# Optimization experiments

Hardware: AMD Instinct MI355X
Metric: run time of the kernel (lower is better)

Reference implementation:

```python
import jax, jax.numpy as jnp
import numpy as np

B, L, H, V = 64, 8, 4096, 50257


def setup_inputs() -> dict:
    key = jax.random.key(0)
    ks = jax.random.split(key, 5)
    return {
        "embedding": jax.random.normal(ks[0], (V, H), jnp.float32) * 0.02,
        "hidden_states": jax.random.normal(ks[1], (B, L, H), jnp.float32),
        "output_position": 7,  # scalar index of the position to sample from
        "temperatures": jax.random.uniform(ks[2], (B,), jnp.float32, 0.5, 1.5),
        "top_ps": jax.random.uniform(ks[3], (B,), jnp.float32, 0.7, 1.0),
        "tops_ks": jax.random.randint(ks[4], (B,), 1, 64),  # top-k in [1,64)
        "embedding_bias": jnp.zeros((V,), jnp.float32),
    }


def reference(embedding, hidden_states, output_position, temperatures, top_ps, tops_ks, embedding_bias):
    # select the output position: [B, H]
    h = hidden_states[:, output_position, :]
    # logits GEMM against tied embedding: [B, V]
    logits = jnp.einsum("bh,vh->bv", h, embedding) + embedding_bias[None, :]
    logits = logits / temperatures[:, None]
    probs = jax.nn.softmax(logits.astype(jnp.float32), axis=-1)

    # descending sort of probabilities
    order = jnp.argsort(-probs, axis=-1)                       # [B, V]
    probs_sort = jnp.take_along_axis(probs, order, axis=-1)    # [B, V]

    # top-p mask: exclusive cumulative sum exceeding top_p
    cum = jnp.cumsum(probs_sort, axis=-1)
    topp_mask = (cum - probs_sort) > top_ps[:, None]
    # top-k mask: rank >= k
    ranks = jnp.arange(V, dtype=tops_ks.dtype)[None, :]
    topk_mask = ranks >= tops_ks[:, None]

    probs_sort = jnp.where(topp_mask | topk_mask, 0.0, probs_sort)
    probs_sort = probs_sort / jnp.sum(probs_sort, axis=-1, keepdims=True)

    # scatter back to original vocab order via inverse permutation
    inv = jnp.argsort(order, axis=-1)
    probs_final = jnp.take_along_axis(probs_sort, inv, axis=-1)  # [B, V]

    # multinomial sampling (1 sample per row)
    logp = jnp.where(probs_final > 0, jnp.log(jnp.maximum(probs_final, 1e-38)), -jnp.inf)
    next_token_ids = jax.random.categorical(jax.random.key(42), logp, axis=-1)
    return next_token_ids
```

## Files before the change

### kernel.cpp

```cpp
#include <hip/hip_runtime.h>
#include <stdint.h>
#include <float.h>
#include <limits.h>


typedef __bf16 bf16x8 __attribute__((ext_vector_type(8)));
typedef float  f32x4  __attribute__((ext_vector_type(4)));

__device__ __forceinline__ void split8v(const float* f, bf16x8& hi, bf16x8& lo) {
#pragma unroll
    for (int e = 0; e < 8; ++e) {
        const __bf16 h = (__bf16)f[e];
        hi[e] = h;
        lo[e] = (__bf16)(f[e] - (float)h);
    }
}
__device__ __forceinline__ void split8(const float* f, uint4& hi, uint4& lo) {
    bf16x8 vh, vl;
    split8v(f, vh, vl);
    hi = __builtin_bit_cast(uint4, vh);
    lo = __builtin_bit_cast(uint4, vl);
}

__global__ __launch_bounds__(256) void prep_h(
    const float* __restrict__ hs, const int* __restrict__ pos_p,
    unsigned short* __restrict__ Ahi, unsigned short* __restrict__ Alo,
    int H, int L)
{
    const int pos = pos_p[0];
    const int tid = blockIdx.x * 256 + threadIdx.x;
    const int b     = tid >> 8;
    const int kbase = (tid & 255) * 16;
    const float* src = hs + ((size_t)b * L + pos) * H + kbase;
    float f[16];
    *(float4*)&f[0]  = *(const float4*)(src);
    *(float4*)&f[4]  = *(const float4*)(src + 4);
    *(float4*)&f[8]  = *(const float4*)(src + 8);
    *(float4*)&f[12] = *(const float4*)(src + 12);

    const int r16 = b >> 4, ll = b & 15;
    const int kc  = kbase >> 5;
    const int lh0 = (kbase >> 3) & 3;
#pragma unroll
    for (int c = 0; c < 2; ++c) {
        uint4 hi, lo;
        split8(f + 8 * c, hi, lo);
        const size_t dst = ((size_t)(r16 * 128 + kc) * 64 + (lh0 + c) * 16 + ll) * 8;
        *(uint4*)&Ahi[dst] = hi;
        *(uint4*)&Alo[dst] = lo;
    }
}

__global__ __launch_bounds__(256) void logits_mfma(
    const float* __restrict__ emb,
    const unsigned short* __restrict__ Ahi,
    const unsigned short* __restrict__ Alo,
    const float* __restrict__ temps,
    const float* __restrict__ bias,
    float*       __restrict__ out,
    int V, int H)
{
    const int tid  = threadIdx.x;
    const int lane = tid & 63;
    const int w    = tid >> 6;
    const int wv0  = blockIdx.x * 128 + w * 32;

    const int ll = lane & 15;
    const int lh = lane >> 4;

    const int NKC = H >> 5;

    const float* bptr[2];
#pragma unroll
    for (int n = 0; n < 2; ++n) {
        int r = wv0 + 16 * n + ll;
        r = (r < V) ? r : (V - 1);
        bptr[n] = emb + (size_t)r * H + lh * 8;
    }

    const size_t aoff = (size_t)lh * 128 + (size_t)ll * 8;

    float4 rb[4][4];
    bf16x8 aih[2][4], ail[2][4];
    f32x4  acc[4][2];
#pragma unroll
    for (int i = 0; i < 4; ++i)
#pragma unroll
        for (int j = 0; j < 2; ++j)
            acc[i][j] = (f32x4){0.f, 0.f, 0.f, 0.f};

#define LOADB(t, bi) do {                                                     \
    if ((t) < NKC) {                                                          \
        _Pragma("unroll")                                                     \
        for (int n = 0; n < 2; ++n) {                                         \
            _Pragma("unroll")                                                 \
            for (int q = 0; q < 2; ++q)                                       \
                rb[bi][n * 2 + q] =                                           \
                    *(const float4*)(bptr[n] + (size_t)(t) * 32 + q * 4);     \
        }                                                                     \
    }                                                                         \
} while (0)

#define LOADA(t, p) do {                                                      \
    if ((t) < NKC) {                                                          \
        _Pragma("unroll")                                                     \
        for (int i = 0; i < 4; ++i) {                                         \
            const size_t ai = aoff + (size_t)i * 65536 + (size_t)(t) * 512;   \
            aih[p][i] = *(const bf16x8*)&Ahi[ai];                             \
            ail[p][i] = *(const bf16x8*)&Alo[ai];                             \
        }                                                                     \
    }                                                                         \
} while (0)

#define COMPUTE(bi, p) do {                                                   \
    bf16x8 fbh[2], fbl[2];                                                    \
    _Pragma("unroll")                                                         \
    for (int n = 0; n < 2; ++n) {                                             \
        float f[8];                                                           \
        *(float4*)&f[0] = rb[bi][2 * n];                                      \
        *(float4*)&f[4] = rb[bi][2 * n + 1];                                  \
        split8v(f, fbh[n], fbl[n]);                                           \
    }                                                                         \
    _Pragma("unroll")                                                         \
    for (int j = 0; j < 2; ++j)                                               \
        _Pragma("unroll")                                                     \
        for (int i = 0; i < 4; ++i) {                                         \
            acc[i][j] = __builtin_amdgcn_mfma_f32_16x16x32_bf16(              \
                ail[p][i], fbh[j], acc[i][j], 0, 0, 0);                       \
            acc[i][j] = __builtin_amdgcn_mfma_f32_16x16x32_bf16(              \
                aih[p][i], fbl[j], acc[i][j], 0, 0, 0);                       \
            acc[i][j] = __builtin_amdgcn_mfma_f32_16x16x32_bf16(              \
                aih[p][i], fbh[j], acc[i][j], 0, 0, 0);                       \
        }                                                                     \
} while (0)

    LOADA(0, 0);
    LOADB(0, 0);
    LOADB(1, 1);
    LOADB(2, 2);

    for (int kb = 0; kb < NKC; kb += 4) {
        LOADB(kb + 3, 3); LOADA(kb + 1, 1); COMPUTE(0, 0);
        LOADB(kb + 4, 0); LOADA(kb + 2, 0); COMPUTE(1, 1);
        LOADB(kb + 5, 1); LOADA(kb + 3, 1); COMPUTE(2, 0);
        LOADB(kb + 6, 2); LOADA(kb + 4, 0); COMPUTE(3, 1);
    }
#undef LOADB
#undef LOADA
#undef COMPUTE

#pragma unroll
    for (int j = 0; j < 2; ++j) {
        const int vv = wv0 + 16 * j + ll;
        if (vv < V) {
            const float bv = bias[vv];
#pragma unroll
            for (int i = 0; i < 4; ++i)
#pragma unroll
                for (int r = 0; r < 4; ++r) {
                    const int b = 16 * i + lh * 4 + r;
                    out[(size_t)b * V + vv] = (acc[i][j][r] + bv) / temps[b];
                }
        }
    }
}

__device__ __forceinline__ uint32_t rotl32(uint32_t x, int d) {
    return (x << d) | (x >> (32 - d));
}

__device__ float jax_gumbel(uint32_t flat) {
    const uint32_t k0 = 0u, k1 = 42u;
    const uint32_t ks[3] = { k0, k1, k0 ^ k1 ^ 0x1BD11BDAu };
    uint32_t x0 = 0u   + ks[0];
    uint32_t x1 = flat + ks[1];
    const int rot[2][4] = { {13, 15, 26, 6}, {17, 29, 16, 24} };
#pragma unroll
    for (int r = 0; r < 5; ++r) {
        const int* rr = rot[r & 1];
#pragma unroll
        for (int j = 0; j < 4; ++j) {
            x0 += x1;
            x1 = rotl32(x1, rr[j]);
            x1 ^= x0;
        }
        x0 += ks[(r + 1) % 3];
        x1 += ks[(r + 2) % 3] + (uint32_t)(r + 1);
    }
    const uint32_t bits = x0 ^ x1;
    const uint32_t fb = (bits >> 9) | 0x3F800000u;
    const float f = __uint_as_float(fb) - 1.0f;
    const float tiny = 1.17549435e-38f;
    float u = __fadd_rn(__fmul_rn(f, 1.0f), tiny);
    u = fmaxf(tiny, u);
    const float l1 = logf(u);
    return -logf(-l1);
}

#define NBINS 4096
#define CAP   2048
#define NKEEP 64

__global__ __launch_bounds__(256) void sample_kernel(
    const float* __restrict__ logits,
    const float* __restrict__ top_ps,
    const int*   __restrict__ top_ks,
    int*         __restrict__ out_ids,
    int V)
{
    const int b = blockIdx.x;
    const int tid = threadIdx.x;
    const float* row = logits + (size_t)b * V;

    __shared__ float swred[4];
    __shared__ int   bins[NBINS];
    __shared__ int   schunk[256];
    __shared__ int   sThrBin, sCnt, sMkeep;
    __shared__ float cval[CAP];
    __shared__ int   cidx[CAP];
    __shared__ float tval[NKEEP];
    __shared__ int   tidxs[NKEEP];

    float m = -INFINITY;
    for (int k = tid; k < V; k += 256) m = fmaxf(m, row[k]);
#pragma unroll
    for (int o = 32; o > 0; o >>= 1) m = fmaxf(m, __shfl_xor(m, o, 64));
    if ((tid & 63) == 0) swred[tid >> 6] = m;
    __syncthreads();
    m = fmaxf(fmaxf(swred[0], swred[1]), fmaxf(swred[2], swred[3]));

    for (int k = tid; k < NBINS; k += 256) bins[k] = 0;
    if (tid == 0) sCnt = 0;
    __syncthreads();

    float s = 0.f;
    for (int k = tid; k < V; k += 256) {
        const float x = row[k];
        s += expf(x - m);
        const float g = m - x;
        int bin = (int)(g * 256.0f);
        if (bin >= NBINS) bin = NBINS - 1;
        atomicAdd(&bins[bin], 1);
    }
#pragma unroll
    for (int o = 32; o > 0; o >>= 1) s += __shfl_xor(s, o, 64);
    __syncthreads();
    if ((tid & 63) == 0) swred[tid >> 6] = s;

    int csum = 0;
#pragma unroll
    for (int k = 0; k < NBINS / 256; ++k) csum += bins[tid * (NBINS / 256) + k];
    schunk[tid] = csum;
    __syncthreads();
    s = swred[0] + swred[1] + swred[2] + swred[3];
    if (tid == 0) {
        int cum = 0, chunk = 255;
        for (int c = 0; c < 256; ++c) {
            if (cum + schunk[c] >= NKEEP) { chunk = c; break; }
            cum += schunk[c];
        }
        int t = NBINS - 1;
        const int base = chunk * (NBINS / 256);
        for (int k = base; k < base + NBINS / 256; ++k) {
            cum += bins[k];
            if (cum >= NKEEP) { t = k; break; }
        }
        sThrBin = t;
    }
    __syncthreads();
    const int thrBin = sThrBin;

    for (int k = tid; k < V; k += 256) {
        const float x = row[k];
        const float g = m - x;
        int bin = (int)(g * 256.0f);
        if (bin >= NBINS) bin = NBINS - 1;
        if (bin <= thrBin) {
            const int p = atomicAdd(&sCnt, 1);
            if (p < CAP) { cval[p] = x; cidx[p] = k; }
        }
    }
    __syncthreads();
    const int C = min(sCnt, CAP);

    for (int i = tid; i < C; i += 256) {
        const float vi = cval[i];
        const int   ii = cidx[i];
        int rank = 0;
        for (int j = 0; j < C; ++j) {
            const float vj = cval[j];
            const int   ij = cidx[j];
            rank += (vj > vi) || (vj == vi && ij < ii);
        }
        if (rank < NKEEP) { tval[rank] = vi; tidxs[rank] = ii; }
    }
    __syncthreads();

    if (tid == 0) {
        const float pb = top_ps[b];
        const int   kk = top_ks[b];
        const int   nk = min(NKEEP, C);
        float cum = 0.f;
        int mk = 0;
        for (int r = 0; r < nk; ++r) {
            const float pr = expf(tval[r] - m) / s;
            cum += pr;
            const float excl = cum - pr;
            if (excl > pb || r >= kk) break;
            ++mk;
        }
        sMkeep = (mk > 0) ? mk : 1;
    }
    __syncthreads();
    const int mkeep = sMkeep;

    if (tid < 64) {
        float sc = -INFINITY;
        int vid = INT_MAX;
        if (tid < mkeep) {
            const int v = tidxs[tid];
            vid = v;
            sc = tval[tid] + jax_gumbel((uint32_t)b * (uint32_t)V + (uint32_t)v);
        }
#pragma unroll
        for (int o = 32; o > 0; o >>= 1) {
            const float os = __shfl_xor(sc, o, 64);
            const int   ov = __shfl_xor(vid, o, 64);
            if (os > sc || (os == sc && ov < vid)) { sc = os; vid = ov; }
        }
        if (tid == 0) out_ids[b] = vid;
    }
}

extern "C" void kernel_launch(void* const* d_in, const int* in_sizes, int n_in,
                              void* d_out, int out_size, void* d_ws, size_t ws_size,
                              hipStream_t stream)
{
    const float* emb   = (const float*)d_in[0];
    const float* hs    = (const float*)d_in[1];
    const int*   pos   = (const int*)d_in[2];
    const float* temps = (const float*)d_in[3];
    const float* tps   = (const float*)d_in[4];
    const int*   tks   = (const int*)d_in[5];
    const float* bias  = (const float*)d_in[6];

    const int B = in_sizes[3];
    const int V = in_sizes[6];
    const int H = (int)((long long)in_sizes[0] / V);
    const int L = (int)((long long)in_sizes[1] / ((long long)B * H));

    float*          logits = (float*)d_ws;
    unsigned short* Ahi    = (unsigned short*)((char*)d_ws + (16u << 20));
    unsigned short* Alo    = Ahi + (size_t)B * H;

    prep_h<<<(B * H) / (16 * 256), 256, 0, stream>>>(hs, pos, Ahi, Alo, H, L);

    const int nblk = (V + 127) / 128;
    logits_mfma<<<nblk, 256, 0, stream>>>(emb, Ahi, Alo, temps, bias,
                                          logits, V, H);

    sample_kernel<<<B, 256, 0, stream>>>(logits, tps, tks, (int*)d_out, V);
}
```

Baseline: 377.2 us.

## Stage embedding rows through swizzled LDS windows with coalesced row loads

Result: slower. 671.3 us (+78.0%).

```diff
diff --git a/kernel.cpp b/kernel.cpp
--- a/kernel.cpp
+++ b/kernel.cpp
@@ -51,7 +51,10 @@
     }
 }
 
-__global__ __launch_bounds__(256) void logits_mfma(
+#define KW   256
+#define TPW  8
+
+__global__ __launch_bounds__(256, 2) void logits_mfma(
     const float* __restrict__ emb,
     const unsigned short* __restrict__ Ahi,
     const unsigned short* __restrict__ Alo,
@@ -60,108 +63,103 @@
     float*       __restrict__ out,
     int V, int H)
 {
+    __shared__ float sB[64 * KW];
+
     const int tid  = threadIdx.x;
     const int lane = tid & 63;
     const int w    = tid >> 6;
-    const int wv0  = blockIdx.x * 128 + w * 32;
+    const int v0   = blockIdx.x * 64;
 
     const int ll = lane & 15;
     const int lh = lane >> 4;
 
-    const int NKC = H >> 5;
-
-    const float* bptr[2];
-#pragma unroll
-    for (int n = 0; n < 2; ++n) {
-        int r = wv0 + 16 * n + ll;
-        r = (r < V) ? r : (V - 1);
-        bptr[n] = emb + (size_t)r * H + lh * 8;
-    }
+    const int NWIN = H / KW;
+    const int NT   = H >> 5;
+
+    const int rl   = 16 * w + ll;
+    const int fswz = ((rl & 7) << 3) ^ (((rl >> 3) & 1) << 2);
 
     const size_t aoff = (size_t)lh * 128 + (size_t)ll * 8;
 
-    float4 rb[4][4];
+    float4 pf[16];
     bf16x8 aih[2][4], ail[2][4];
-    f32x4  acc[4][2];
-#pragma unroll
-    for (int i = 0; i < 4; ++i)
-#pragma unroll
-        for (int j = 0; j < 2; ++j)
-            acc[i][j] = (f32x4){0.f, 0.f, 0.f, 0.f};
-
-#define LOADB(t, bi) do {                                                     \
-    if ((t) < NKC) {                                                          \
-        _Pragma("unroll")                                                     \
-        for (int n = 0; n < 2; ++n) {                                         \
-            _Pragma("unroll")                                                 \
-            for (int q = 0; q < 2; ++q)                                       \
-                rb[bi][n * 2 + q] =                                           \
-                    *(const float4*)(bptr[n] + (size_t)(t) * 32 + q * 4);     \
-        }                                                                     \
+    f32x4  acc[4];
+#pragma unroll
+    for (int i = 0; i < 4; ++i) acc[i] = (f32x4){0.f, 0.f, 0.f, 0.f};
+
+#define LOADW(win) do {                                                       \
+    const int wb = (win) * KW;                                                \
+    _Pragma("unroll")                                                         \
+    for (int i = 0; i < 16; ++i) {                                            \
+        int rg = v0 + 16 * w + i;                                             \
+        rg = (rg < V) ? rg : (V - 1);                                         \
+        pf[i] = *(const float4*)(emb + (size_t)rg * H + wb + lane * 4);       \
     }                                                                         \
 } while (0)
 
-#define LOADA(t, p) do {                                                      \
-    if ((t) < NKC) {                                                          \
-        _Pragma("unroll")                                                     \
-        for (int i = 0; i < 4; ++i) {                                         \
-            const size_t ai = aoff + (size_t)i * 65536 + (size_t)(t) * 512;   \
-            aih[p][i] = *(const bf16x8*)&Ahi[ai];                             \
-            ail[p][i] = *(const bf16x8*)&Alo[ai];                             \
-        }                                                                     \
+#define STOREW() do {                                                         \
+    _Pragma("unroll")                                                         \
+    for (int i = 0; i < 16; ++i) {                                            \
+        const int row = 16 * w + i;                                           \
+        const int sz  = ((i & 7) << 3) ^ (((i >> 3) & 1) << 2);               \
+        *(float4*)&sB[row * KW + ((lane * 4) ^ sz)] = pf[i];                  \
     }                                                                         \
 } while (0)
 
-#define COMPUTE(bi, p) do {                                                   \
-    bf16x8 fbh[2], fbl[2];                                                    \
+#define LOADA(t, p) do {                                                      \
     _Pragma("unroll")                                                         \
-    for (int n = 0; n < 2; ++n) {                                             \
-        float f[8];                                                           \
-        *(float4*)&f[0] = rb[bi][2 * n];                                      \
-        *(float4*)&f[4] = rb[bi][2 * n + 1];                                  \
-        split8v(f, fbh[n], fbl[n]);                                           \
+    for (int i = 0; i < 4; ++i) {                                             \
+        const size_t ai = aoff + (size_t)i * 65536 + (size_t)(t) * 512;       \
+        aih[p][i] = *(const bf16x8*)&Ahi[ai];                                 \
+        ail[p][i] = *(const bf16x8*)&Alo[ai];                                 \
     }                                                                         \
-    _Pragma("unroll")                                                         \
-    for (int j = 0; j < 2; ++j)                                               \
-        _Pragma("unroll")                                                     \
-        for (int i = 0; i < 4; ++i) {                                         \
-            acc[i][j] = __builtin_amdgcn_mfma_f32_16x16x32_bf16(              \
-                ail[p][i], fbh[j], acc[i][j], 0, 0, 0);                       \
-            acc[i][j] = __builtin_amdgcn_mfma_f32_16x16x32_bf16(              \
-                aih[p][i], fbl[j], acc[i][j], 0, 0, 0);                       \
-            acc[i][j] = __builtin_amdgcn_mfma_f32_16x16x32_bf16(              \
-                aih[p][i], fbh[j], acc[i][j], 0, 0, 0);                       \
-        }                                                                     \
 } while (0)
 
+    LOADW(0);
+    STOREW();
     LOADA(0, 0);
-    LOADB(0, 0);
-    LOADB(1, 1);
-    LOADB(2, 2);
-
-    for (int kb = 0; kb < NKC; kb += 4) {
-        LOADB(kb + 3, 3); LOADA(kb + 1, 1); COMPUTE(0, 0);
-        LOADB(kb + 4, 0); LOADA(kb + 2, 0); COMPUTE(1, 1);
-        LOADB(kb + 5, 1); LOADA(kb + 3, 1); COMPUTE(2, 0);
-        LOADB(kb + 6, 2); LOADA(kb + 4, 0); COMPUTE(3, 1);
-    }
-#undef LOADB
+
+    for (int win = 0; win < NWIN; ++win) {
+        if (win + 1 < NWIN) LOADW(win + 1);
+#pragma unroll
+        for (int kt = 0; kt < TPW; ++kt) {
+            const int t = win * TPW + kt;
+            const int p = t & 1;
+            if (t + 1 < NT) LOADA(t + 1, p ^ 1);
+
+            const int kb = kt * 32 + lh * 8;
+            float f[8];
+            *(float4*)&f[0] = *(const float4*)&sB[rl * KW + ((kb)     ^ fswz)];
+            *(float4*)&f[4] = *(const float4*)&sB[rl * KW + ((kb + 4) ^ fswz)];
+            bf16x8 fbh, fbl;
+            split8v(f, fbh, fbl);
+
+#pragma unroll
+            for (int i = 0; i < 4; ++i) {
+                acc[i] = __builtin_amdgcn_mfma_f32_16x16x32_bf16(
+                    ail[p][i], fbh, acc[i], 0, 0, 0);
+                acc[i] = __builtin_amdgcn_mfma_f32_16x16x32_bf16(
+                    aih[p][i], fbl, acc[i], 0, 0, 0);
+                acc[i] = __builtin_amdgcn_mfma_f32_16x16x32_bf16(
+                    aih[p][i], fbh, acc[i], 0, 0, 0);
+            }
+        }
+        if (win + 1 < NWIN) STOREW();
+    }
+#undef LOADW
+#undef STOREW
 #undef LOADA
-#undef COMPUTE
-
-#pragma unroll
-    for (int j = 0; j < 2; ++j) {
-        const int vv = wv0 + 16 * j + ll;
-        if (vv < V) {
-            const float bv = bias[vv];
-#pragma unroll
-            for (int i = 0; i < 4; ++i)
-#pragma unroll
-                for (int r = 0; r < 4; ++r) {
-                    const int b = 16 * i + lh * 4 + r;
-                    out[(size_t)b * V + vv] = (acc[i][j][r] + bv) / temps[b];
-                }
-        }
+
+    const int vv = v0 + 16 * w + ll;
+    if (vv < V) {
+        const float bv = bias[vv];
+#pragma unroll
+        for (int i = 0; i < 4; ++i)
+#pragma unroll
+            for (int r = 0; r < 4; ++r) {
+                const int b = 16 * i + lh * 4 + r;
+                out[(size_t)b * V + vv] = (acc[i][r] + bv) / temps[b];
+            }
     }
 }
 
@@ -355,7 +353,7 @@
 
     prep_h<<<(B * H) / (16 * 256), 256, 0, stream>>>(hs, pos, Ahi, Alo, H, L);
 
-    const int nblk = (V + 127) / 128;
+    const int nblk = (V + 63) / 64;
     logits_mfma<<<nblk, 256, 0, stream>>>(emb, Ahi, Alo, temps, bias,
                                           logits, V, H);
 
```
